# Kernel optimization log

Hardware: AMD Instinct MI355X
Metric: run time of the kernel (lower is better)

The kernel has to match this reference:

```python
import jax, jax.numpy as jnp
import numpy as np
from jax import lax

V, H, L, F = 50304, 512, 6, 2048
SKIP_INTERVAL = 1
B, S = 4, 1024


def layer_norm(x, w, b, eps=1e-5):
    mu = jnp.mean(x, axis=-1, keepdims=True)
    var = jnp.mean(jnp.square(x - mu), axis=-1, keepdims=True)
    return (x - mu) * lax.rsqrt(var + eps) * w + b


def setup_inputs() -> dict:
    key = jax.random.key(0)
    ks = jax.random.split(key, 8)
    s = 0.02
    return {
        "input_ids": jax.random.randint(ks[0], (B, S), 0, V, dtype=jnp.int64),
        "embed_in": jax.random.normal(ks[1], (V, H), jnp.float32) * s,
        "hp_w": jax.random.normal(ks[2], (H, H), jnp.float32) * s,
        "hp_b": jnp.zeros((H,), jnp.float32),
        "ln_w": jnp.ones((L, H), jnp.float32),
        "ln_b": jnp.zeros((L, H), jnp.float32),
        "W1": jax.random.normal(ks[3], (L, H, F), jnp.float32) * s,
        "b1": jnp.zeros((L, F), jnp.float32),
        "W2": jax.random.normal(ks[4], (L, F, H), jnp.float32) * s,
        "b2": jnp.zeros((L, H), jnp.float32),
        "ln_f_w": jnp.ones((H,), jnp.float32),
        "ln_f_b": jnp.zeros((H,), jnp.float32),
        "embed_out_w": jax.random.normal(ks[5], (V, H), jnp.float32) * s,
    }


def _stack(h, ln_w, ln_b, W1, b1, W2, b2):
    # scan over L layers; each is pre-LN residual MLP: h + gelu(LN(h) @ W1 + b1) @ W2 + b2
    def step(h, p):
        lw, lb, w1, bb1, w2, bb2 = p
        y = layer_norm(h, lw, lb)
        h = h + jnp.dot(jax.nn.gelu(jnp.dot(y, w1) + bb1), w2) + bb2
        return h, None
    h, _ = lax.scan(step, h, (ln_w, ln_b, W1, b1, W2, b2))
    return h


def reference(input_ids, embed_in, hp_w, hp_b, ln_w, ln_b, W1, b1, W2, b2, ln_f_w, ln_f_b, embed_out_w):
    # forward_selective with attention_mask=None and stateless layers is
    # position-independent, so the token loop vectorizes exactly to [B,S,H].
    h = embed_in[input_ids]  # [B,S,H] gather
    h = _stack(h, ln_w, ln_b, W1, b1, W2, b2)
    for _ in range(SKIP_INTERVAL):
        h = jnp.dot(h, hp_w.T) + hp_b  # hidden_proj
        h = _stack(h, ln_w, ln_b, W1, b1, W2, b2)
    normed = layer_norm(h, ln_f_w, ln_f_b)
    logits = jnp.dot(normed, embed_out_w.T)  # [B,S,V]
    final_hidden = h[:, -1, :]  # [B,H]
    return logits, final_hidden
```

## Files before the change

kernel.cpp:

```cpp
#include <hip/hip_runtime.h>
#include <hip/hip_bf16.h>
#include <cstdint>

using bf16 = __hip_bfloat16;
typedef __bf16 bf16x8 __attribute__((ext_vector_type(8)));
typedef float f32x4 __attribute__((ext_vector_type(4)));

constexpr int Hd = 512;
constexpr int Ld = 6;
constexpr int Fd = 2048;
constexpr int Vd = 50304;
constexpr int Vpad = 50432;
constexpr int Md = 4096;

__device__ __forceinline__ unsigned short f2b(float x) {
  return __builtin_bit_cast(unsigned short, __float2bfloat16(x));
}

__device__ __forceinline__ float gelu_tanh(float x) {
  const float c = 0.7978845608028654f;
  float x3 = x * x * x;
  return 0.5f * x * (1.0f + tanhf(c * (x + 0.044715f * x3)));
}

__device__ __forceinline__ void load16_lds(const bf16* g, bf16* l) {
  __builtin_amdgcn_global_load_lds(
      (const __attribute__((address_space(1))) void*)g,
      (__attribute__((address_space(3))) void*)l, 16, 0, 0);
}

__global__ __launch_bounds__(256) void cast8(const float* __restrict__ in,
                                             bf16* __restrict__ out, int n8) {
  int i = blockIdx.x * 256 + threadIdx.x;
  if (i >= n8) return;
  const float4* p = (const float4*)in;
  float4 a = p[2 * i], b = p[2 * i + 1];
  uint4 o = {(unsigned)f2b(a.x) | ((unsigned)f2b(a.y) << 16),
             (unsigned)f2b(a.z) | ((unsigned)f2b(a.w) << 16),
             (unsigned)f2b(b.x) | ((unsigned)f2b(b.y) << 16),
             (unsigned)f2b(b.z) | ((unsigned)f2b(b.w) << 16)};
  ((uint4*)out)[i] = o;
}

__global__ __launch_bounds__(256) void zero16(bf16* __restrict__ p, int n8) {
  int i = blockIdx.x * 256 + threadIdx.x;
  if (i < n8) ((uint4*)p)[i] = uint4{0, 0, 0, 0};
}

__global__ void transpose_cast(const float* __restrict__ in, bf16* __restrict__ out,
                               int R, int C) {
  __shared__ float tile[32][33];
  int l = blockIdx.z;
  in += (size_t)l * R * C;
  out += (size_t)l * R * C;
  int c0 = blockIdx.x * 32, r0 = blockIdx.y * 32;
#pragma unroll
  for (int i = 0; i < 4; i++) {
    int r = r0 + threadIdx.y + i * 8;
    tile[threadIdx.y + i * 8][threadIdx.x] = in[(size_t)r * C + c0 + threadIdx.x];
  }
  __syncthreads();
#pragma unroll
  for (int i = 0; i < 4; i++) {
    int c = c0 + threadIdx.y + i * 8;
    out[(size_t)c * R + r0 + threadIdx.x] = (bf16)tile[threadIdx.x][threadIdx.y + i * 8];
  }
}

__global__ void gather_embed(const int* __restrict__ ids, const float* __restrict__ emb,
                             float* __restrict__ h) {
  int row = blockIdx.x;
  int id = ids[row];
  const float4* src = (const float4*)(emb + (size_t)id * Hd);
  float4* dst = (float4*)(h + (size_t)row * Hd);
  dst[threadIdx.x] = src[threadIdx.x];
}

template <int MODE>
__global__ __launch_bounds__(256) void ln_rows(
    const float* __restrict__ h, const float* __restrict__ p0,
    const float* __restrict__ p1, const float* __restrict__ fb,
    const float* __restrict__ w, const float* __restrict__ b,
    float* __restrict__ hout, bf16* __restrict__ y) {
  int row = blockIdx.x * 4 + (threadIdx.x >> 6);
  int lane = threadIdx.x & 63;
  size_t base = (size_t)row * Hd + lane * 8;
  float xv[8];
  if constexpr (MODE == 0) {
    *(float4*)&xv[0] = *(const float4*)(h + base);
    *(float4*)&xv[4] = *(const float4*)(h + base + 4);
  } else {
    float4 q0 = *(const float4*)(p0 + base), q1 = *(const float4*)(p0 + base + 4);
    float4 r0 = *(const float4*)(p1 + base), r1 = *(const float4*)(p1 + base + 4);
    float4 f0 = *(const float4*)(fb + lane * 8), f1 = *(const float4*)(fb + lane * 8 + 4);
    xv[0] = q0.x + r0.x + f0.x; xv[1] = q0.y + r0.y + f0.y;
    xv[2] = q0.z + r0.z + f0.z; xv[3] = q0.w + r0.w + f0.w;
    xv[4] = q1.x + r1.x + f1.x; xv[5] = q1.y + r1.y + f1.y;
    xv[6] = q1.z + r1.z + f1.z; xv[7] = q1.w + r1.w + f1.w;
    if constexpr (MODE == 1) {
      float4 a0 = *(const float4*)(h + base), a1 = *(const float4*)(h + base + 4);
      xv[0] += a0.x; xv[1] += a0.y; xv[2] += a0.z; xv[3] += a0.w;
      xv[4] += a1.x; xv[5] += a1.y; xv[6] += a1.z; xv[7] += a1.w;
    }
    *(float4*)(hout + base) = make_float4(xv[0], xv[1], xv[2], xv[3]);
    *(float4*)(hout + base + 4) = make_float4(xv[4], xv[5], xv[6], xv[7]);
  }
  float s = 0.f;
#pragma unroll
  for (int j = 0; j < 8; j++) s += xv[j];
#pragma unroll
  for (int off = 1; off < 64; off <<= 1) s += __shfl_xor(s, off);
  float mu = s * (1.0f / 512.0f);
  float s2 = 0.f;
#pragma unroll
  for (int j = 0; j < 8; j++) {
    xv[j] -= mu;
    s2 += xv[j] * xv[j];
  }
#pragma unroll
  for (int off = 1; off < 64; off <<= 1) s2 += __shfl_xor(s2, off);
  float scale = rsqrtf(s2 * (1.0f / 512.0f) + 1e-5f);
  float o[8];
#pragma unroll
  for (int j = 0; j < 8; j++) {
    float wj = w[lane * 8 + j], bj = b[lane * 8 + j];
    o[j] = xv[j] * scale * wj + bj;
  }
  uint4 pk = {(unsigned)f2b(o[0]) | ((unsigned)f2b(o[1]) << 16),
              (unsigned)f2b(o[2]) | ((unsigned)f2b(o[3]) << 16),
              (unsigned)f2b(o[4]) | ((unsigned)f2b(o[5]) << 16),
              (unsigned)f2b(o[6]) | ((unsigned)f2b(o[7]) << 16)};
  *(uint4*)(y + base) = pk;
}

__global__ __launch_bounds__(256) void finish2(
    const float* __restrict__ p0, const float* __restrict__ p1,
    const float* __restrict__ fb, float* __restrict__ h, bf16* __restrict__ hbf) {
  int i = blockIdx.x * 256 + threadIdx.x;
  size_t base = (size_t)i * 8;
  int col = (int)(base & 511);
  float x[8];
#pragma unroll
  for (int j = 0; j < 8; j += 4) {
    float4 a = *(const float4*)(h + base + j);
    float4 q = *(const float4*)(p0 + base + j);
    float4 r = *(const float4*)(p1 + base + j);
    float4 f = *(const float4*)(fb + col + j);
    x[j] = a.x + q.x + r.x + f.x; x[j + 1] = a.y + q.y + r.y + f.y;
    x[j + 2] = a.z + q.z + r.z + f.z; x[j + 3] = a.w + q.w + r.w + f.w;
    *(float4*)(h + base + j) = make_float4(x[j], x[j + 1], x[j + 2], x[j + 3]);
  }
  uint4 pk = {(unsigned)f2b(x[0]) | ((unsigned)f2b(x[1]) << 16),
              (unsigned)f2b(x[2]) | ((unsigned)f2b(x[3]) << 16),
              (unsigned)f2b(x[4]) | ((unsigned)f2b(x[5]) << 16),
              (unsigned)f2b(x[6]) | ((unsigned)f2b(x[7]) << 16)};
  *(uint4*)(hbf + base) = pk;
}

template <int EPI, int BN, bool MSWZ>
__global__ __launch_bounds__(256) void gemm_bt(
    const bf16* __restrict__ A, const bf16* __restrict__ Bt,
    const float* __restrict__ bias, float* __restrict__ outF,
    bf16* __restrict__ outB, int M, int N, int Klen, int lda, int ldb) {
  constexpr int ASZ = 128 * 32;
  constexpr int BSZ = BN * 32;
  constexpr int TILE = ASZ + BSZ;
  __shared__ bf16 lds[3 * TILE];
  const int tid = threadIdx.x;
  const int wave = tid >> 6;
  const int lane = tid & 63;
  constexpr int NF = BN / 32;
  const int wm = (wave >> 1) * 64;
  const int wn = (wave & 1) * (BN / 2);

  int bm, bn;
  if constexpr (MSWZ) {
    const int per = gridDim.x >> 3;
    const int wg = (blockIdx.x & 7) * per + (blockIdx.x >> 3);
    const int nM = M >> 7;
    bm = wg & (nM - 1);
    bn = wg / nM;
  } else {
    bn = blockIdx.x;
    bm = blockIdx.y;
  }
  const int rowA0 = bm * 128;
  const int rowB0 = bn * BN;
  const int k0 = blockIdx.z * Klen;

  const bf16* srcA[2];
#pragma unroll
  for (int r = 0; r < 2; r++) {
    int c = (r * 4 + wave) * 64 + lane;
    srcA[r] = A + (size_t)(rowA0 + (c >> 2)) * lda + k0 + (c & 3) * 8;
  }
  const bf16* srcB[BN / 64];
#pragma unroll
  for (int r = 0; r < BN / 64; r++) {
    int c = (r * 4 + wave) * 64 + lane;
    srcB[r] = Bt + (size_t)(rowB0 + (c >> 2)) * ldb + k0 + (c & 3) * 8;
  }

  f32x4 acc[4][NF];
#pragma unroll
  for (int i = 0; i < 4; i++)
#pragma unroll
    for (int j = 0; j < NF; j++) acc[i][j] = (f32x4){0.f, 0.f, 0.f, 0.f};

  const int fr = lane & 15;
  const int ko = (lane >> 4) * 8;

  auto STAGE = [&](int slot) {
    bf16* dst = lds + slot * TILE;
#pragma unroll
    for (int r = 0; r < 2; r++) {
      load16_lds(srcA[r], dst + (r * 4 + wave) * 512);
      srcA[r] += 32;
    }
#pragma unroll
    for (int r = 0; r < BN / 64; r++) {
      load16_lds(srcB[r], dst + ASZ + (r * 4 + wave) * 512);
      srcB[r] += 32;
    }
  };

  STAGE(0);
  STAGE(1);
  const int nIter = Klen >> 5;
  int cur = 0, stg = 2;
  for (int it = 0; it < nIter; ++it) {
    if (it < nIter - 1) {
      if constexpr (BN == 64)
        asm volatile("s_waitcnt vmcnt(3)" ::: "memory");
      else
        asm volatile("s_waitcnt vmcnt(4)" ::: "memory");
    } else {
      asm volatile("s_waitcnt vmcnt(0)" ::: "memory");
    }
    __builtin_amdgcn_s_barrier();
    __builtin_amdgcn_sched_barrier(0);
    if (it + 2 < nIter) STAGE(stg);
    const bf16* lA = lds + cur * TILE;
    const bf16* lB = lA + ASZ;
    bf16x8 af[4], bfr[NF];
#pragma unroll
    for (int f = 0; f < 4; f++)
      af[f] = *(const bf16x8*)(lA + (wm + f * 16 + fr) * 32 + ko);
#pragma unroll
    for (int f = 0; f < NF; f++)
      bfr[f] = *(const bf16x8*)(lB + (wn + f * 16 + fr) * 32 + ko);
#pragma unroll
    for (int i = 0; i < 4; i++)
#pragma unroll
      for (int j = 0; j < NF; j++)
        acc[i][j] = __builtin_amdgcn_mfma_f32_16x16x32_bf16(af[i], bfr[j], acc[i][j], 0, 0, 0);
    cur = (cur == 2) ? 0 : cur + 1;
    stg = (stg == 2) ? 0 : stg + 1;
  }

  if constexpr (EPI == 4) outF += (size_t)blockIdx.z * M * N;
  const int orow = (lane >> 4) * 4;
  const int ocol = lane & 15;
#pragma unroll
  for (int i = 0; i < 4; i++) {
#pragma unroll
    for (int j = 0; j < NF; j++) {
      int row0 = rowA0 + wm + i * 16 + orow;
      int col = rowB0 + wn + j * 16 + ocol;
#pragma unroll
      for (int q = 0; q < 4; q++) {
        float v = acc[i][j][q];
        size_t idx = (size_t)(row0 + q) * N + col;
        if constexpr (EPI == 0) {
          outB[idx] = (bf16)gelu_tanh(v + bias[col]);
        } else {
          outF[idx] = v;
        }
      }
    }
  }
}

template <int EPI, bool MSWZ>
__global__ __launch_bounds__(512) void gemm_bt256(
    const bf16* __restrict__ A, const bf16* __restrict__ Bt,
    const float* __restrict__ bias, float* __restrict__ outF,
    bf16* __restrict__ outB, int M, int N, int lda, int ldb) {
  constexpr int ASZ = 256 * 32;
  constexpr int BSZ = 128 * 32;
  constexpr int TILE = ASZ + BSZ;
  __shared__ bf16 lds[3 * TILE];
  const int tid = threadIdx.x;
  const int wave = tid >> 6;
  const int lane = tid & 63;
  const int wm = (wave >> 1) * 64;
  const int wn = (wave & 1) * 64;

  int bm, bn;
  if constexpr (MSWZ) {
    const int per = gridDim.x >> 3;
    const int wg = (blockIdx.x & 7) * per + (blockIdx.x >> 3);
    const int nM = M >> 8;
    bm = wg & (nM - 1);
    bn = wg / nM;
  } else {
    bn = blockIdx.x;
    bm = blockIdx.y;
  }
  const int rowA0 = bm * 256;
  const int rowB0 = bn * 128;

  const bf16* srcA[2];
#pragma unroll
  for (int r = 0; r < 2; r++) {
    int c = r * 512 + tid;
    srcA[r] = A + (size_t)(rowA0 + (c >> 2)) * lda + (c & 3) * 8;
  }
  int cB = tid;
  const bf16* srcB = Bt + (size_t)(rowB0 + (cB >> 2)) * ldb + (cB & 3) * 8;

  f32x4 acc[4][4];
#pragma unroll
  for (int i = 0; i < 4; i++)
#pragma unroll
    for (int j = 0; j < 4; j++) acc[i][j] = (f32x4){0.f, 0.f, 0.f, 0.f};

  const int fr = lane & 15;
  const int ko = (lane >> 4) * 8;

  auto STAGE = [&](int slot) {
    bf16* dst = lds + slot * TILE;
#pragma unroll
    for (int r = 0; r < 2; r++) {
      load16_lds(srcA[r], dst + (r * 512 + tid) * 8);
      srcA[r] += 32;
    }
    load16_lds(srcB, dst + ASZ + tid * 8);
    srcB += 32;
  };

  STAGE(0);
  STAGE(1);
  const int nIter = 512 >> 5;
  int cur = 0, stg = 2;
  for (int it = 0; it < nIter; ++it) {
    if (it < nIter - 1)
      asm volatile("s_waitcnt vmcnt(3)" ::: "memory");
    else
      asm volatile("s_waitcnt vmcnt(0)" ::: "memory");
    __builtin_amdgcn_s_barrier();
    __builtin_amdgcn_sched_barrier(0);
    if (it + 2 < nIter) STAGE(stg);
    const bf16* lA = lds + cur * TILE;
    const bf16* lB = lA + ASZ;
    bf16x8 af[4], bfr[4];
#pragma unroll
    for (int f = 0; f < 4; f++)
      af[f] = *(const bf16x8*)(lA + (wm + f * 16 + fr) * 32 + ko);
#pragma unroll
    for (int f = 0; f < 4; f++)
      bfr[f] = *(const bf16x8*)(lB + (wn + f * 16 + fr) * 32 + ko);
#pragma unroll
    for (int i = 0; i < 4; i++)
#pragma unroll
      for (int j = 0; j < 4; j++)
        acc[i][j] = __builtin_amdgcn_mfma_f32_16x16x32_bf16(af[i], bfr[j], acc[i][j], 0, 0, 0);
    cur = (cur == 2) ? 0 : cur + 1;
    stg = (stg == 2) ? 0 : stg + 1;
  }

  const int orow = (lane >> 4) * 4;
  const int ocol = lane & 15;
#pragma unroll
  for (int i = 0; i < 4; i++) {
#pragma unroll
    for (int j = 0; j < 4; j++) {
      int row0 = rowA0 + wm + i * 16 + orow;
      int col = rowB0 + wn + j * 16 + ocol;
#pragma unroll
      for (int q = 0; q < 4; q++) {
        float v = acc[i][j][q];
        size_t idx = (size_t)(row0 + q) * N + col;
        if constexpr (EPI == 0) {
          outB[idx] = (bf16)gelu_tanh(v + bias[col]);
        } else {
          outF[idx] = v;
        }
      }
    }
  }
}

__global__ __launch_bounds__(512, 1) void gemm_logits(
    const bf16* __restrict__ A, const bf16* __restrict__ Bt,
    float* __restrict__ outF, int M, int N, int lda, int ldb) {
  constexpr int ASZ = 256 * 32;
  constexpr int BSZ = 256 * 32;
  constexpr int TILE = ASZ + BSZ;
  __shared__ bf16 lds[3 * TILE];
  const int tid = threadIdx.x;
  const int wave = tid >> 6;
  const int lane = tid & 63;
  const int wm = (wave >> 2) * 128;
  const int wn = (wave & 3) * 64;

  const int per = gridDim.x >> 3;
  const int wg = (blockIdx.x & 7) * per + (blockIdx.x >> 3);
  const int bm = wg & 15;
  const int bn = wg >> 4;
  const int rowA0 = bm * 256;
  const int rowB0 = bn * 256;

  const bf16* srcA[2];
  const bf16* srcB[2];
#pragma unroll
  for (int r = 0; r < 2; r++) {
    int c = r * 512 + tid;
    srcA[r] = A + (size_t)(rowA0 + (c >> 2)) * lda + (c & 3) * 8;
    srcB[r] = Bt + (size_t)(rowB0 + (c >> 2)) * ldb + (c & 3) * 8;
  }

  f32x4 acc[8][4];
#pragma unroll
  for (int i = 0; i < 8; i++)
#pragma unroll
    for (int j = 0; j < 4; j++) acc[i][j] = (f32x4){0.f, 0.f, 0.f, 0.f};

  const int fr = lane & 15;
  const int ko = (lane >> 4) * 8;

  auto STAGE = [&](int slot) {
    bf16* dst = lds + slot * TILE;
#pragma unroll
    for (int r = 0; r < 2; r++) {
      load16_lds(srcA[r], dst + (r * 512 + tid) * 8);
      srcA[r] += 32;
      load16_lds(srcB[r], dst + ASZ + (r * 512 + tid) * 8);
      srcB[r] += 32;
    }
  };

  STAGE(0);
  STAGE(1);
  const int nIter = 512 >> 5;
  int cur = 0, stg = 2;
  for (int it = 0; it < nIter; ++it) {
    if (it < nIter - 1)
      asm volatile("s_waitcnt vmcnt(4)" ::: "memory");
    else
      asm volatile("s_waitcnt vmcnt(0)" ::: "memory");
    __builtin_amdgcn_s_barrier();
    __builtin_amdgcn_sched_barrier(0);
    if (it + 2 < nIter) STAGE(stg);
    const bf16* lA = lds + cur * TILE;
    const bf16* lB = lA + ASZ;
    bf16x8 af[8], bfr[4];
#pragma unroll
    for (int f = 0; f < 8; f++)
      af[f] = *(const bf16x8*)(lA + (wm + f * 16 + fr) * 32 + ko);
#pragma unroll
    for (int f = 0; f < 4; f++)
      bfr[f] = *(const bf16x8*)(lB + (wn + f * 16 + fr) * 32 + ko);
#pragma unroll
    for (int i = 0; i < 8; i++)
#pragma unroll
      for (int j = 0; j < 4; j++)
        acc[i][j] = __builtin_amdgcn_mfma_f32_16x16x32_bf16(af[i], bfr[j], acc[i][j], 0, 0, 0);
    cur = (cur == 2) ? 0 : cur + 1;
    stg = (stg == 2) ? 0 : stg + 1;
  }

  const int orow = (lane >> 4) * 4;
  const int ocol = lane & 15;
#pragma unroll
  for (int i = 0; i < 8; i++) {
#pragma unroll
    for (int j = 0; j < 4; j++) {
      int row0 = rowA0 + wm + i * 16 + orow;
      int col = rowB0 + wn + j * 16 + ocol;
      if (col < N) {
#pragma unroll
        for (int q = 0; q < 4; q++)
          outF[(size_t)(row0 + q) * N + col] = acc[i][j][q];
      }
    }
  }
}

__global__ void tail_copy(const float* __restrict__ h, float* __restrict__ out) {
  int t = blockIdx.x * 256 + threadIdx.x;
  int b = t >> 9, k = t & 511;
  out[t] = h[((size_t)(b * 1024 + 1023)) * Hd + k];
}

extern "C" void kernel_launch(void* const* d_in, const int* in_sizes, int n_in,
                              void* d_out, int out_size, void* d_ws, size_t ws_size,
                              hipStream_t stream) {
  const int* ids = (const int*)d_in[0];
  const float* emb = (const float*)d_in[1];
  const float* hp_w = (const float*)d_in[2];
  const float* hp_b = (const float*)d_in[3];
  const float* ln_w = (const float*)d_in[4];
  const float* ln_b = (const float*)d_in[5];
  const float* W1 = (const float*)d_in[6];
  const float* b1 = (const float*)d_in[7];
  const float* W2 = (const float*)d_in[8];
  const float* b2 = (const float*)d_in[9];
  const float* lnf_w = (const float*)d_in[10];
  const float* lnf_b = (const float*)d_in[11];
  const float* eow = (const float*)d_in[12];
  float* out = (float*)d_out;

  char* ws = (char*)d_ws;
  float* h = (float*)(ws);
  bf16* ybf = (bf16*)(ws + (8u << 20));
  bf16* abf = (bf16*)(ws + (12u << 20));
  bf16* W1t = (bf16*)(ws + (28u << 20));
  bf16* W2t = (bf16*)(ws + (40u << 20));
  bf16* hpwB = (bf16*)(ws + (52u << 20));
  bf16* eowB = (bf16*)(ws + (53u << 20));

  float* p0 = out;
  float* p1 = out + (size_t)Md * Hd;

  cast8<<<dim3(Vd * Hd / 8 / 256), dim3(256), 0, stream>>>(eow, eowB, Vd * Hd / 8);
  zero16<<<dim3((Vpad - Vd) * Hd / 8 / 256), dim3(256), 0, stream>>>(
      eowB + (size_t)Vd * Hd, (Vpad - Vd) * Hd / 8);
  cast8<<<dim3(Hd * Hd / 8 / 256), dim3(256), 0, stream>>>(hp_w, hpwB, Hd * Hd / 8);
  transpose_cast<<<dim3(Fd / 32, Hd / 32, Ld), dim3(32, 8), 0, stream>>>(W1, W1t, Hd, Fd);
  transpose_cast<<<dim3(Hd / 32, Fd / 32, Ld), dim3(32, 8), 0, stream>>>(W2, W2t, Fd, Hd);

  gather_embed<<<dim3(Md), dim3(128), 0, stream>>>(ids, emb, h);

  auto layer = [&](int l, int mode, const float* fb, const float* lw, const float* lb) {
    if (mode == 0)
      ln_rows<0><<<dim3(Md / 4), dim3(256), 0, stream>>>(h, p0, p1, fb, lw, lb, h, ybf);
    else if (mode == 1)
      ln_rows<1><<<dim3(Md / 4), dim3(256), 0, stream>>>(h, p0, p1, fb, lw, lb, h, ybf);
    else
      ln_rows<2><<<dim3(Md / 4), dim3(256), 0, stream>>>(h, p0, p1, fb, lw, lb, h, ybf);
    gemm_bt256<0, false><<<dim3(Fd / 128, Md / 256), dim3(512), 0, stream>>>(
        ybf, W1t + (size_t)l * Fd * Hd, b1 + (size_t)l * Fd, (float*)nullptr, abf,
        Md, Fd, Hd, Hd);
    gemm_bt<4, 128, false><<<dim3(Hd / 128, Md / 128, 2), dim3(256), 0, stream>>>(
        abf, W2t + (size_t)l * Hd * Fd, (const float*)nullptr, p0, (bf16*)nullptr,
        Md, Hd, Fd / 2, Fd, Fd);
  };

  layer(0, 0, nullptr, ln_w, ln_b);
  for (int l = 1; l < Ld; l++)
    layer(l, 1, b2 + (size_t)(l - 1) * Hd, ln_w + (size_t)l * Hd, ln_b + (size_t)l * Hd);
  finish2<<<dim3(Md * Hd / 8 / 256), dim3(256), 0, stream>>>(
      p0, p1, b2 + (size_t)(Ld - 1) * Hd, h, ybf);

  gemm_bt<4, 128, false><<<dim3(Hd / 128, Md / 128, 2), dim3(256), 0, stream>>>(
      ybf, hpwB, (const float*)nullptr, p0, (bf16*)nullptr, Md, Hd, Hd / 2, Hd, Hd);

  layer(0, 2, hp_b, ln_w, ln_b);
  for (int l = 1; l < Ld; l++)
    layer(l, 1, b2 + (size_t)(l - 1) * Hd, ln_w + (size_t)l * Hd, ln_b + (size_t)l * Hd);

  ln_rows<1><<<dim3(Md / 4), dim3(256), 0, stream>>>(
      h, p0, p1, b2 + (size_t)(Ld - 1) * Hd, lnf_w, lnf_b, h, ybf);
  gemm_logits<<<dim3((Vpad / 256) * (Md / 256)), dim3(512), 0, stream>>>(
      ybf, eowB, out, Md, Vd, Hd, Hd);

  tail_copy<<<dim3(8), dim3(256), 0, stream>>>(h, out + (size_t)Md * Vd);
}
```

Before: 984.1 us.

## XOR-swizzle LDS layout and deepen K-tile to 64 in MLP GEMMs

The FFN and projection GEMMs now stage 64-wide K tiles instead of 32-wide, which halves the number of barrier/wait iterations per tile. Global loads use an XOR-swizzled column chunk so LDS fragment reads avoid bank conflicts. The logits GEMM gets the same swizzle at its 32-wide K. The unused MSWZ and BN template options are removed. Shared-memory use per block roughly doubles for the MLP GEMMs, which can lower occupancy.

```diff
diff --git a/kernel.cpp b/kernel.cpp
--- a/kernel.cpp
+++ b/kernel.cpp
@@ -157,114 +157,100 @@
   *(uint4*)(hbf + base) = pk;
 }
 
-template <int EPI, int BN, bool MSWZ>
+
+template <int EPI>
 __global__ __launch_bounds__(256) void gemm_bt(
     const bf16* __restrict__ A, const bf16* __restrict__ Bt,
     const float* __restrict__ bias, float* __restrict__ outF,
     bf16* __restrict__ outB, int M, int N, int Klen, int lda, int ldb) {
-  constexpr int ASZ = 128 * 32;
-  constexpr int BSZ = BN * 32;
-  constexpr int TILE = ASZ + BSZ;
+  constexpr int ASZ = 128 * 64;
+  constexpr int TILE = 2 * ASZ;
   __shared__ bf16 lds[3 * TILE];
   const int tid = threadIdx.x;
   const int wave = tid >> 6;
   const int lane = tid & 63;
-  constexpr int NF = BN / 32;
   const int wm = (wave >> 1) * 64;
-  const int wn = (wave & 1) * (BN / 2);
-
-  int bm, bn;
-  if constexpr (MSWZ) {
-    const int per = gridDim.x >> 3;
-    const int wg = (blockIdx.x & 7) * per + (blockIdx.x >> 3);
-    const int nM = M >> 7;
-    bm = wg & (nM - 1);
-    bn = wg / nM;
-  } else {
-    bn = blockIdx.x;
-    bm = blockIdx.y;
-  }
+  const int wn = (wave & 1) * 64;
+
+  const int bn = blockIdx.x;
+  const int bm = blockIdx.y;
   const int rowA0 = bm * 128;
-  const int rowB0 = bn * BN;
+  const int rowB0 = bn * 128;
   const int k0 = blockIdx.z * Klen;
 
-  const bf16* srcA[2];
-#pragma unroll
-  for (int r = 0; r < 2; r++) {
-    int c = (r * 4 + wave) * 64 + lane;
-    srcA[r] = A + (size_t)(rowA0 + (c >> 2)) * lda + k0 + (c & 3) * 8;
-  }
-  const bf16* srcB[BN / 64];
-#pragma unroll
-  for (int r = 0; r < BN / 64; r++) {
-    int c = (r * 4 + wave) * 64 + lane;
-    srcB[r] = Bt + (size_t)(rowB0 + (c >> 2)) * ldb + k0 + (c & 3) * 8;
-  }
-
-  f32x4 acc[4][NF];
+  const bf16* srcA[4];
+  const bf16* srcB[4];
+#pragma unroll
+  for (int r = 0; r < 4; r++) {
+    int c = r * 256 + tid;
+    int row = c >> 3, d = c & 7;
+    int cw = d ^ (row & 7);
+    srcA[r] = A + (size_t)(rowA0 + row) * lda + k0 + cw * 8;
+    srcB[r] = Bt + (size_t)(rowB0 + row) * ldb + k0 + cw * 8;
+  }
+
+  f32x4 acc[4][4];
 #pragma unroll
   for (int i = 0; i < 4; i++)
 #pragma unroll
-    for (int j = 0; j < NF; j++) acc[i][j] = (f32x4){0.f, 0.f, 0.f, 0.f};
+    for (int j = 0; j < 4; j++) acc[i][j] = (f32x4){0.f, 0.f, 0.f, 0.f};
 
   const int fr = lane & 15;
-  const int ko = (lane >> 4) * 8;
+  const int hi = lane >> 4;
+  const int swz = fr & 7;
 
   auto STAGE = [&](int slot) {
     bf16* dst = lds + slot * TILE;
 #pragma unroll
-    for (int r = 0; r < 2; r++) {
+    for (int r = 0; r < 4; r++) {
       load16_lds(srcA[r], dst + (r * 4 + wave) * 512);
-      srcA[r] += 32;
-    }
-#pragma unroll
-    for (int r = 0; r < BN / 64; r++) {
+      srcA[r] += 64;
       load16_lds(srcB[r], dst + ASZ + (r * 4 + wave) * 512);
-      srcB[r] += 32;
+      srcB[r] += 64;
     }
   };
 
   STAGE(0);
   STAGE(1);
-  const int nIter = Klen >> 5;
+  const int nIter = Klen >> 6;
   int cur = 0, stg = 2;
   for (int it = 0; it < nIter; ++it) {
-    if (it < nIter - 1) {
-      if constexpr (BN == 64)
-        asm volatile("s_waitcnt vmcnt(3)" ::: "memory");
-      else
-        asm volatile("s_waitcnt vmcnt(4)" ::: "memory");
-    } else {
+    if (it < nIter - 1)
+      asm volatile("s_waitcnt vmcnt(8)" ::: "memory");
+    else
       asm volatile("s_waitcnt vmcnt(0)" ::: "memory");
-    }
     __builtin_amdgcn_s_barrier();
     __builtin_amdgcn_sched_barrier(0);
     if (it + 2 < nIter) STAGE(stg);
     const bf16* lA = lds + cur * TILE;
     const bf16* lB = lA + ASZ;
-    bf16x8 af[4], bfr[NF];
-#pragma unroll
-    for (int f = 0; f < 4; f++)
-      af[f] = *(const bf16x8*)(lA + (wm + f * 16 + fr) * 32 + ko);
-#pragma unroll
-    for (int f = 0; f < NF; f++)
-      bfr[f] = *(const bf16x8*)(lB + (wn + f * 16 + fr) * 32 + ko);
-#pragma unroll
-    for (int i = 0; i < 4; i++)
-#pragma unroll
-      for (int j = 0; j < NF; j++)
-        acc[i][j] = __builtin_amdgcn_mfma_f32_16x16x32_bf16(af[i], bfr[j], acc[i][j], 0, 0, 0);
+#pragma unroll
+    for (int ks = 0; ks < 2; ks++) {
+      bf16x8 af[4], bfr[4];
+#pragma unroll
+      for (int f = 0; f < 4; f++) {
+        int rowa = wm + f * 16 + fr;
+        af[f] = *(const bf16x8*)(lA + rowa * 64 + ((ks * 4 + hi) ^ swz) * 8);
+        int rowb = wn + f * 16 + fr;
+        bfr[f] = *(const bf16x8*)(lB + rowb * 64 + ((ks * 4 + hi) ^ swz) * 8);
+      }
+#pragma unroll
+      for (int i = 0; i < 4; i++)
+#pragma unroll
+        for (int j = 0; j < 4; j++)
+          acc[i][j] = __builtin_amdgcn_mfma_f32_16x16x32_bf16(af[i], bfr[j], acc[i][j], 0, 0, 0);
+    }
     cur = (cur == 2) ? 0 : cur + 1;
     stg = (stg == 2) ? 0 : stg + 1;
   }
 
   if constexpr (EPI == 4) outF += (size_t)blockIdx.z * M * N;
-  const int orow = (lane >> 4) * 4;
-  const int ocol = lane & 15;
+  const int orow = hi * 4;
+  const int ocol = fr;
 #pragma unroll
   for (int i = 0; i < 4; i++) {
 #pragma unroll
-    for (int j = 0; j < NF; j++) {
+    for (int j = 0; j < 4; j++) {
       int row0 = rowA0 + wm + i * 16 + orow;
       int col = rowB0 + wn + j * 16 + ocol;
 #pragma unroll
@@ -281,13 +267,13 @@
   }
 }
 
-template <int EPI, bool MSWZ>
+template <int EPI>
 __global__ __launch_bounds__(512) void gemm_bt256(
     const bf16* __restrict__ A, const bf16* __restrict__ Bt,
     const float* __restrict__ bias, float* __restrict__ outF,
     bf16* __restrict__ outB, int M, int N, int lda, int ldb) {
-  constexpr int ASZ = 256 * 32;
-  constexpr int BSZ = 128 * 32;
+  constexpr int ASZ = 256 * 64;
+  constexpr int BSZ = 128 * 64;
   constexpr int TILE = ASZ + BSZ;
   __shared__ bf16 lds[3 * TILE];
   const int tid = threadIdx.x;
@@ -296,28 +282,27 @@
   const int wm = (wave >> 1) * 64;
   const int wn = (wave & 1) * 64;
 
-  int bm, bn;
-  if constexpr (MSWZ) {
-    const int per = gridDim.x >> 3;
-    const int wg = (blockIdx.x & 7) * per + (blockIdx.x >> 3);
-    const int nM = M >> 8;
-    bm = wg & (nM - 1);
-    bn = wg / nM;
-  } else {
-    bn = blockIdx.x;
-    bm = blockIdx.y;
-  }
+  const int bn = blockIdx.x;
+  const int bm = blockIdx.y;
   const int rowA0 = bm * 256;
   const int rowB0 = bn * 128;
 
-  const bf16* srcA[2];
+  const bf16* srcA[4];
+#pragma unroll
+  for (int r = 0; r < 4; r++) {
+    int c = r * 512 + tid;
+    int row = c >> 3, d = c & 7;
+    int cw = d ^ (row & 7);
+    srcA[r] = A + (size_t)(rowA0 + row) * lda + cw * 8;
+  }
+  const bf16* srcB[2];
 #pragma unroll
   for (int r = 0; r < 2; r++) {
     int c = r * 512 + tid;
-    srcA[r] = A + (size_t)(rowA0 + (c >> 2)) * lda + (c & 3) * 8;
-  }
-  int cB = tid;
-  const bf16* srcB = Bt + (size_t)(rowB0 + (cB >> 2)) * ldb + (cB & 3) * 8;
+    int row = c >> 3, d = c & 7;
+    int cw = d ^ (row & 7);
+    srcB[r] = Bt + (size_t)(rowB0 + row) * ldb + cw * 8;
+  }
 
   f32x4 acc[4][4];
 #pragma unroll
@@ -326,26 +311,30 @@
     for (int j = 0; j < 4; j++) acc[i][j] = (f32x4){0.f, 0.f, 0.f, 0.f};
 
   const int fr = lane & 15;
-  const int ko = (lane >> 4) * 8;
+  const int hi = lane >> 4;
+  const int swz = fr & 7;
 
   auto STAGE = [&](int slot) {
     bf16* dst = lds + slot * TILE;
 #pragma unroll
+    for (int r = 0; r < 4; r++) {
+      load16_lds(srcA[r], dst + (r * 8 + wave) * 512);
+      srcA[r] += 64;
+    }
+#pragma unroll
     for (int r = 0; r < 2; r++) {
-      load16_lds(srcA[r], dst + (r * 512 + tid) * 8);
-      srcA[r] += 32;
-    }
-    load16_lds(srcB, dst + ASZ + tid * 8);
-    srcB += 32;
+      load16_lds(srcB[r], dst + ASZ + (r * 8 + wave) * 512);
+      srcB[r] += 64;
+    }
   };
 
   STAGE(0);
   STAGE(1);
-  const int nIter = 512 >> 5;
+  const int nIter = 512 >> 6;
   int cur = 0, stg = 2;
   for (int it = 0; it < nIter; ++it) {
     if (it < nIter - 1)
-      asm volatile("s_waitcnt vmcnt(3)" ::: "memory");
+      asm volatile("s_waitcnt vmcnt(6)" ::: "memory");
     else
       asm volatile("s_waitcnt vmcnt(0)" ::: "memory");
     __builtin_amdgcn_s_barrier();
@@ -353,24 +342,28 @@
     if (it + 2 < nIter) STAGE(stg);
     const bf16* lA = lds + cur * TILE;
     const bf16* lB = lA + ASZ;
-    bf16x8 af[4], bfr[4];
-#pragma unroll
-    for (int f = 0; f < 4; f++)
-      af[f] = *(const bf16x8*)(lA + (wm + f * 16 + fr) * 32 + ko);
-#pragma unroll
-    for (int f = 0; f < 4; f++)
-      bfr[f] = *(const bf16x8*)(lB + (wn + f * 16 + fr) * 32 + ko);
-#pragma unroll
-    for (int i = 0; i < 4; i++)
-#pragma unroll
-      for (int j = 0; j < 4; j++)
-        acc[i][j] = __builtin_amdgcn_mfma_f32_16x16x32_bf16(af[i], bfr[j], acc[i][j], 0, 0, 0);
+#pragma unroll
+    for (int ks = 0; ks < 2; ks++) {
+      bf16x8 af[4], bfr[4];
+#pragma unroll
+      for (int f = 0; f < 4; f++) {
+        int rowa = wm + f * 16 + fr;
+        af[f] = *(const bf16x8*)(lA + rowa * 64 + ((ks * 4 + hi) ^ swz) * 8);
+        int rowb = wn + f * 16 + fr;
+        bfr[f] = *(const bf16x8*)(lB + rowb * 64 + ((ks * 4 + hi) ^ swz) * 8);
+      }
+#pragma unroll
+      for (int i = 0; i < 4; i++)
+#pragma unroll
+        for (int j = 0; j < 4; j++)
+          acc[i][j] = __builtin_amdgcn_mfma_f32_16x16x32_bf16(af[i], bfr[j], acc[i][j], 0, 0, 0);
+    }
     cur = (cur == 2) ? 0 : cur + 1;
     stg = (stg == 2) ? 0 : stg + 1;
   }
 
-  const int orow = (lane >> 4) * 4;
-  const int ocol = lane & 15;
+  const int orow = hi * 4;
+  const int ocol = fr;
 #pragma unroll
   for (int i = 0; i < 4; i++) {
 #pragma unroll
@@ -395,8 +388,7 @@
     const bf16* __restrict__ A, const bf16* __restrict__ Bt,
     float* __restrict__ outF, int M, int N, int lda, int ldb) {
   constexpr int ASZ = 256 * 32;
-  constexpr int BSZ = 256 * 32;
-  constexpr int TILE = ASZ + BSZ;
+  constexpr int TILE = 2 * ASZ;
   __shared__ bf16 lds[3 * TILE];
   const int tid = threadIdx.x;
   const int wave = tid >> 6;
@@ -416,8 +408,10 @@
 #pragma unroll
   for (int r = 0; r < 2; r++) {
     int c = r * 512 + tid;
-    srcA[r] = A + (size_t)(rowA0 + (c >> 2)) * lda + (c & 3) * 8;
-    srcB[r] = Bt + (size_t)(rowB0 + (c >> 2)) * ldb + (c & 3) * 8;
+    int row = c >> 2, d = c & 3;
+    int cw = d ^ ((row >> 1) & 3);
+    srcA[r] = A + (size_t)(rowA0 + row) * lda + cw * 8;
+    srcB[r] = Bt + (size_t)(rowB0 + row) * ldb + cw * 8;
   }
 
   f32x4 acc[8][4];
@@ -427,15 +421,16 @@
     for (int j = 0; j < 4; j++) acc[i][j] = (f32x4){0.f, 0.f, 0.f, 0.f};
 
   const int fr = lane & 15;
-  const int ko = (lane >> 4) * 8;
+  const int hi = lane >> 4;
+  const int sw32 = (fr >> 1) & 3;
 
   auto STAGE = [&](int slot) {
     bf16* dst = lds + slot * TILE;
 #pragma unroll
     for (int r = 0; r < 2; r++) {
-      load16_lds(srcA[r], dst + (r * 512 + tid) * 8);
+      load16_lds(srcA[r], dst + (r * 8 + wave) * 512);
       srcA[r] += 32;
-      load16_lds(srcB[r], dst + ASZ + (r * 512 + tid) * 8);
+      load16_lds(srcB[r], dst + ASZ + (r * 8 + wave) * 512);
       srcB[r] += 32;
     }
   };
@@ -456,11 +451,15 @@
     const bf16* lB = lA + ASZ;
     bf16x8 af[8], bfr[4];
 #pragma unroll
-    for (int f = 0; f < 8; f++)
-      af[f] = *(const bf16x8*)(lA + (wm + f * 16 + fr) * 32 + ko);
-#pragma unroll
-    for (int f = 0; f < 4; f++)
-      bfr[f] = *(const bf16x8*)(lB + (wn + f * 16 + fr) * 32 + ko);
+    for (int f = 0; f < 8; f++) {
+      int rowa = wm + f * 16 + fr;
+      af[f] = *(const bf16x8*)(lA + rowa * 32 + (hi ^ sw32) * 8);
+    }
+#pragma unroll
+    for (int f = 0; f < 4; f++) {
+      int rowb = wn + f * 16 + fr;
+      bfr[f] = *(const bf16x8*)(lB + rowb * 32 + (hi ^ sw32) * 8);
+    }
 #pragma unroll
     for (int i = 0; i < 8; i++)
 #pragma unroll
@@ -470,8 +469,8 @@
     stg = (stg == 2) ? 0 : stg + 1;
   }
 
-  const int orow = (lane >> 4) * 4;
-  const int ocol = lane & 15;
+  const int orow = hi * 4;
+  const int ocol = fr;
 #pragma unroll
   for (int i = 0; i < 8; i++) {
 #pragma unroll
@@ -539,10 +538,10 @@
       ln_rows<1><<<dim3(Md / 4), dim3(256), 0, stream>>>(h, p0, p1, fb, lw, lb, h, ybf);
     else
       ln_rows<2><<<dim3(Md / 4), dim3(256), 0, stream>>>(h, p0, p1, fb, lw, lb, h, ybf);
-    gemm_bt256<0, false><<<dim3(Fd / 128, Md / 256), dim3(512), 0, stream>>>(
+    gemm_bt256<0><<<dim3(Fd / 128, Md / 256), dim3(512), 0, stream>>>(
         ybf, W1t + (size_t)l * Fd * Hd, b1 + (size_t)l * Fd, (float*)nullptr, abf,
         Md, Fd, Hd, Hd);
-    gemm_bt<4, 128, false><<<dim3(Hd / 128, Md / 128, 2), dim3(256), 0, stream>>>(
+    gemm_bt<4><<<dim3(Hd / 128, Md / 128, 2), dim3(256), 0, stream>>>(
         abf, W2t + (size_t)l * Hd * Fd, (const float*)nullptr, p0, (bf16*)nullptr,
         Md, Hd, Fd / 2, Fd, Fd);
   };
@@ -553,7 +552,7 @@
   finish2<<<dim3(Md * Hd / 8 / 256), dim3(256), 0, stream>>>(
       p0, p1, b2 + (size_t)(Ld - 1) * Hd, h, ybf);
 
-  gemm_bt<4, 128, false><<<dim3(Hd / 128, Md / 128, 2), dim3(256), 0, stream>>>(
+  gemm_bt<4><<<dim3(Hd / 128, Md / 128, 2), dim3(256), 0, stream>>>(
       ybf, hpwB, (const float*)nullptr, p0, (bf16*)nullptr, Md, Hd, Hd / 2, Hd, Hd);
 
   layer(0, 2, hp_b, ln_w, ln_b);
```

Result: faster. 944.0 us (-4.1%).
